# Kernel tuning notes

Hardware: AMD Instinct MI355X
Metric: run time of the kernel (lower is better)

Reference implementation:

```python
import jax, jax.numpy as jnp
import numpy as np

N_NODES = 50000
N_EDGES = 800000
N_GRAPHS = 500
IN_DIM = 128
HID = 96
OUT_DIM = 64


def _lin(k, fan_in, fan_out):
    return jax.random.normal(k, (fan_in, fan_out), jnp.float32) / np.float32(np.sqrt(fan_in))


def setup_inputs() -> dict:
    key = jax.random.key(0)
    ks = jax.random.split(key, 12)
    x = jax.random.normal(ks[0], (N_NODES, IN_DIM), jnp.float32)
    edge_index = jax.random.randint(ks[1], (2, N_EDGES), 0, N_NODES)
    batch = jnp.sort(jax.random.randint(ks[2], (N_NODES,), 0, N_GRAPHS))
    return {
        "x": x,
        "edge_index": edge_index,
        "batch": batch,
        # GCN conv weights (first: in->hid, rest: hid->hid)
        "W0": _lin(ks[3], IN_DIM, HID), "b0": jnp.zeros((HID,), jnp.float32),
        "W1": _lin(ks[4], HID, HID),    "b1": jnp.zeros((HID,), jnp.float32),
        "W2": _lin(ks[5], HID, HID),    "b2": jnp.zeros((HID,), jnp.float32),
        # jumping-knowledge 'cat' projection: 3*hid -> hid
        "Wjk": _lin(ks[6], 3 * HID, HID), "bjk": jnp.zeros((HID,), jnp.float32),
        # fc_o MLP: hid -> hid -> out
        "Wm1": _lin(ks[7], HID, HID),   "bm1": jnp.zeros((HID,), jnp.float32),
        "Wm2": _lin(ks[8], HID, OUT_DIM), "bm2": jnp.zeros((OUT_DIM,), jnp.float32),
    }


def reference(x, edge_index, batch, W0, b0, W1, b1, W2, b2, Wjk, bjk, Wm1, bm1, Wm2, bm2):
    n = x.shape[0]
    loop = jnp.arange(n, dtype=edge_index.dtype)
    src = jnp.concatenate([edge_index[0], loop])  # [E+N] with self-loops
    dst = jnp.concatenate([edge_index[1], loop])
    # symmetric GCN normalization: D^{-1/2} (A+I) D^{-1/2}
    deg = jax.ops.segment_sum(jnp.ones_like(dst, x.dtype), dst, num_segments=n)
    dinv = jax.lax.rsqrt(jnp.maximum(deg, 1.0))  # deg >= 1 with self-loops
    norm = dinv[src] * dinv[dst]  # [E+N]

    def gcn_conv(h, W, b):
        m = (h @ W)[src] * norm[:, None]                      # gather + scale
        return jax.ops.segment_sum(m, dst, num_segments=n) + b  # scatter-add

    h1 = jax.nn.relu(gcn_conv(x, W0, b0))
    h2 = jax.nn.relu(gcn_conv(h1, W1, b1))
    h3 = jax.nn.relu(gcn_conv(h2, W2, b2))
    # JK 'cat' + final linear (PyG BasicGNN lin)
    h = jnp.concatenate([h1, h2, h3], axis=-1) @ Wjk + bjk    # [N, HID]
    # global add pooling over graphs
    emb_o = jax.ops.segment_sum(h, batch, num_segments=N_GRAPHS)  # [G, HID]
    # fc_o MLP (eval: dropout/identity-batchnorm omitted)
    pred_o = jax.nn.relu(emb_o @ Wm1 + bm1) @ Wm2 + bm2       # [G, OUT]
    return pred_o
```

## Files before the change

### kernel.cpp

```cpp
#include <hip/hip_runtime.h>
#include <hip/hip_fp16.h>

#define NN 50000
#define NE 800000
#define NG 500
#define IND 128
#define HD 96
#define OD 64

#define SCAN_CHUNK 2048
#define SCAN_BLOCKS ((NN + SCAN_CHUNK - 1) / SCAN_CHUNK)


__global__ void zero_k(int* __restrict__ cnt) {
  int i = blockIdx.x * 256 + threadIdx.x;
  if (i < NN) cnt[i] = 0;
}

__global__ void hist_k(const int* __restrict__ dst, int* __restrict__ cnt,
                       int* __restrict__ rank) {
  int i0 = (blockIdx.x * 256 + threadIdx.x) * 8;
  if (i0 + 8 <= NE) {
    int4 d0 = *reinterpret_cast<const int4*>(&dst[i0]);
    int4 d1 = *reinterpret_cast<const int4*>(&dst[i0 + 4]);
    int4 r0, r1;
    r0.x = atomicAdd(&cnt[d0.x], 1);
    r0.y = atomicAdd(&cnt[d0.y], 1);
    r0.z = atomicAdd(&cnt[d0.z], 1);
    r0.w = atomicAdd(&cnt[d0.w], 1);
    r1.x = atomicAdd(&cnt[d1.x], 1);
    r1.y = atomicAdd(&cnt[d1.y], 1);
    r1.z = atomicAdd(&cnt[d1.z], 1);
    r1.w = atomicAdd(&cnt[d1.w], 1);
    *reinterpret_cast<int4*>(&rank[i0]) = r0;
    *reinterpret_cast<int4*>(&rank[i0 + 4]) = r1;
  } else {
    for (int i = i0; i < NE; i++) rank[i] = atomicAdd(&cnt[dst[i]], 1);
  }
}

__global__ void gstart_k(const int* __restrict__ batch, int* __restrict__ gstart) {
  int n = blockIdx.x * 256 + threadIdx.x;
  if (n >= NN) return;
  if (n == 0) {
    for (int g = 0; g <= batch[0]; g++) gstart[g] = 0;
    for (int g = batch[NN - 1] + 1; g <= NG; g++) gstart[g] = NN;
  } else {
    int b0 = batch[n - 1], b1 = batch[n];
    for (int g = b0 + 1; g <= b1; g++) gstart[g] = n;
  }
}

__global__ __launch_bounds__(256) void scan_part_k(const int* __restrict__ cnt,
                                                   int* __restrict__ bsum,
                                                   float* __restrict__ dinv) {
  __shared__ int ts[256];
  const int tid = threadIdx.x;
  const int base = blockIdx.x * SCAN_CHUNK + tid * 8;
  int s = 0;
#pragma unroll
  for (int j = 0; j < 8; j++) {
    int idx = base + j;
    if (idx < NN) {
      int c = cnt[idx];
      s += c;
      dinv[idx] = rsqrtf((float)(c + 1));
    }
  }
  ts[tid] = s;
  __syncthreads();
  for (int off = 128; off > 0; off >>= 1) {
    if (tid < off) ts[tid] += ts[tid + off];
    __syncthreads();
  }
  if (tid == 0) bsum[blockIdx.x] = ts[0];
}

__global__ __launch_bounds__(64) void scan_top_k(const int* __restrict__ bsum,
                                                 int* __restrict__ boff,
                                                 int* __restrict__ row_ptr) {
  int tid = threadIdx.x;
  int v = (tid < SCAN_BLOCKS) ? bsum[tid] : 0;
  for (int off = 1; off < 64; off <<= 1) {
    int u = __shfl_up(v, off);
    if (tid >= off) v += u;
  }
  if (tid < SCAN_BLOCKS) boff[tid] = v - bsum[tid];
  if (tid == 0) row_ptr[NN] = NE;
}

__global__ __launch_bounds__(256) void scan_fin_k(const int* __restrict__ cnt,
                                                  const int* __restrict__ boff,
                                                  int* __restrict__ row_ptr) {
  __shared__ int ts[256];
  const int tid = threadIdx.x;
  const int base = blockIdx.x * SCAN_CHUNK + tid * 8;
  int v[8];
  int s = 0;
#pragma unroll
  for (int j = 0; j < 8; j++) {
    int idx = base + j;
    v[j] = (idx < NN) ? cnt[idx] : 0;
    s += v[j];
  }
  ts[tid] = s;
  __syncthreads();
  for (int off = 1; off < 256; off <<= 1) {
    int t = (tid >= off) ? ts[tid - off] : 0;
    __syncthreads();
    ts[tid] += t;
    __syncthreads();
  }
  int run = ((tid == 0) ? 0 : ts[tid - 1]) + boff[blockIdx.x];
#pragma unroll
  for (int j = 0; j < 8; j++) {
    int idx = base + j;
    if (idx < NN) row_ptr[idx] = run;
    run += v[j];
  }
}

__global__ void fill_k(const int* __restrict__ src, const int* __restrict__ dst,
                       const int* __restrict__ row_ptr, const int* __restrict__ rank,
                       int* __restrict__ col) {
  int i0 = (blockIdx.x * 256 + threadIdx.x) * 8;
  if (i0 + 8 <= NE) {
    int4 d0 = *reinterpret_cast<const int4*>(&dst[i0]);
    int4 d1 = *reinterpret_cast<const int4*>(&dst[i0 + 4]);
    int4 s0 = *reinterpret_cast<const int4*>(&src[i0]);
    int4 s1 = *reinterpret_cast<const int4*>(&src[i0 + 4]);
    int4 r0 = *reinterpret_cast<const int4*>(&rank[i0]);
    int4 r1 = *reinterpret_cast<const int4*>(&rank[i0 + 4]);
    int p0 = row_ptr[d0.x], p1 = row_ptr[d0.y], p2 = row_ptr[d0.z], p3 = row_ptr[d0.w];
    int p4 = row_ptr[d1.x], p5 = row_ptr[d1.y], p6 = row_ptr[d1.z], p7 = row_ptr[d1.w];
    col[p0 + r0.x] = s0.x * (HD * 2);
    col[p1 + r0.y] = s0.y * (HD * 2);
    col[p2 + r0.z] = s0.z * (HD * 2);
    col[p3 + r0.w] = s0.w * (HD * 2);
    col[p4 + r1.x] = s1.x * (HD * 2);
    col[p5 + r1.y] = s1.y * (HD * 2);
    col[p6 + r1.z] = s1.z * (HD * 2);
    col[p7 + r1.w] = s1.w * (HD * 2);
  } else {
    for (int i = i0; i < NE; i++)
      col[row_ptr[dst[i]] + rank[i]] = src[i] * (HD * 2);
  }
}

template <int K, typename T>
__global__ __launch_bounds__(256) void gemm_scale_k(const T* __restrict__ h,
                                                    const float* __restrict__ W,
                                                    const float* __restrict__ dinv,
                                                    __half* __restrict__ g) {
  __shared__ float hsT[32][66];
  __shared__ __attribute__((aligned(16))) float ws[32][100];
  const int tid = threadIdx.x;
  const int rowg = tid >> 3;
  const int colg = tid & 7;
  const int row0 = blockIdx.x * 64;

  float acc[2][12];
#pragma unroll
  for (int i = 0; i < 2; i++)
#pragma unroll
    for (int j = 0; j < 12; j++) acc[i][j] = 0.f;

  for (int k0 = 0; k0 < K; k0 += 32) {
    if constexpr (sizeof(T) == 4) {
#pragma unroll
      for (int lin = tid; lin < 512; lin += 256) {
        int r = lin >> 3, q = lin & 7;
        int grow = row0 + r;
        float4 v = make_float4(0.f, 0.f, 0.f, 0.f);
        if (grow < NN)
          v = *reinterpret_cast<const float4*>(&h[(long)grow * K + k0 + 4 * q]);
        hsT[4 * q + 0][r] = v.x;
        hsT[4 * q + 1][r] = v.y;
        hsT[4 * q + 2][r] = v.z;
        hsT[4 * q + 3][r] = v.w;
      }
    } else {
      {
        int r = tid >> 2, q = tid & 3;
        int grow = row0 + r;
        if (grow < NN) {
          int4 raw = *reinterpret_cast<const int4*>(
              reinterpret_cast<const __half*>(h) + (long)grow * K + k0 + 8 * q);
          const __half2* hp = reinterpret_cast<const __half2*>(&raw);
#pragma unroll
          for (int t = 0; t < 4; t++) {
            float2 f = __half22float2(hp[t]);
            hsT[8 * q + 2 * t + 0][r] = f.x;
            hsT[8 * q + 2 * t + 1][r] = f.y;
          }
        } else {
#pragma unroll
          for (int t = 0; t < 8; t++) hsT[8 * q + t][r] = 0.f;
        }
      }
    }
#pragma unroll
    for (int lin = tid; lin < 768; lin += 256) {
      int kk = lin / 24, c4 = lin - kk * 24;
      *reinterpret_cast<float4*>(&ws[kk][4 * c4]) =
          *reinterpret_cast<const float4*>(&W[(long)(k0 + kk) * HD + 4 * c4]);
    }
    __syncthreads();
#pragma unroll 8
    for (int k = 0; k < 32; k++) {
      float2 a = *reinterpret_cast<const float2*>(&hsT[k][2 * rowg]);
      float4 w0 = *reinterpret_cast<const float4*>(&ws[k][12 * colg]);
      float4 w1 = *reinterpret_cast<const float4*>(&ws[k][12 * colg + 4]);
      float4 w2 = *reinterpret_cast<const float4*>(&ws[k][12 * colg + 8]);
      float wv[12] = {w0.x, w0.y, w0.z, w0.w, w1.x, w1.y, w1.z, w1.w,
                      w2.x, w2.y, w2.z, w2.w};
      float av[2] = {a.x, a.y};
#pragma unroll
      for (int i = 0; i < 2; i++)
#pragma unroll
        for (int j = 0; j < 12; j++) acc[i][j] = fmaf(av[i], wv[j], acc[i][j]);
    }
    __syncthreads();
  }
#pragma unroll
  for (int i = 0; i < 2; i++) {
    int row = row0 + 2 * rowg + i;
    if (row < NN) {
      float dv = dinv[row];
      __half2 hh[6];
#pragma unroll
      for (int q = 0; q < 6; q++)
        hh[q] = __floats2half2_rn(acc[i][2 * q] * dv, acc[i][2 * q + 1] * dv);
      __half* go = g + (long)row * HD + 12 * colg;
      *reinterpret_cast<float2*>(go) = *reinterpret_cast<float2*>(&hh[0]);
      *reinterpret_cast<float2*>(go + 4) = *reinterpret_cast<float2*>(&hh[2]);
      *reinterpret_cast<float2*>(go + 8) = *reinterpret_cast<float2*>(&hh[4]);
    }
  }
}

__global__ __launch_bounds__(256) void gather_k(const __half* __restrict__ g,
                                                const int* __restrict__ row_ptr,
                                                const int* __restrict__ col,
                                                const float* __restrict__ dinv,
                                                const float* __restrict__ bias,
                                                __half* __restrict__ hout) {
  int d = blockIdx.x * 4 + (threadIdx.x >> 6);
  int lane = threadIdx.x & 63;
  if (d >= NN) return;
  const bool active = (lane < 48);
  const int s = active ? (lane / 12) : 0;
  const int c = active ? (lane % 12) : 0;
  const int cofs = 16 * c;
  const char* gb = reinterpret_cast<const char*>(g);
  const int own = d * (HD * 2);

  float acc[8];
#pragma unroll
  for (int k = 0; k < 8; k++) acc[k] = 0.f;

  {
    float4 raw = *reinterpret_cast<const float4*>(gb + own + cofs);
    const __half2* hp = reinterpret_cast<const __half2*>(&raw);
    float m = (active && s == 0) ? 1.f : 0.f;
#pragma unroll
    for (int q = 0; q < 4; q++) {
      float2 f = __half22float2(hp[q]);
      acc[2 * q + 0] = fmaf(m, f.x, acc[2 * q + 0]);
      acc[2 * q + 1] = fmaf(m, f.y, acc[2 * q + 1]);
    }
  }

  int e = row_ptr[d];
  const int end = row_ptr[d + 1];
  while (e < end) {
    int cnt = end - e; if (cnt > 64) cnt = 64;
    int cid = (lane < cnt) ? col[e + lane] : own;
    int j = 0;
    for (; j + 16 <= cnt; j += 16) {
      int o0 = __shfl(cid, j + s);
      int o1 = __shfl(cid, j + 4 + s);
      int o2 = __shfl(cid, j + 8 + s);
      int o3 = __shfl(cid, j + 12 + s);
      float4 r0 = *reinterpret_cast<const float4*>(gb + o0 + cofs);
      float4 r1 = *reinterpret_cast<const float4*>(gb + o1 + cofs);
      float4 r2 = *reinterpret_cast<const float4*>(gb + o2 + cofs);
      float4 r3 = *reinterpret_cast<const float4*>(gb + o3 + cofs);
      const __half2* h0 = reinterpret_cast<const __half2*>(&r0);
      const __half2* h1 = reinterpret_cast<const __half2*>(&r1);
      const __half2* h2 = reinterpret_cast<const __half2*>(&r2);
      const __half2* h3 = reinterpret_cast<const __half2*>(&r3);
#pragma unroll
      for (int q = 0; q < 4; q++) {
        float2 f0 = __half22float2(h0[q]);
        float2 f1 = __half22float2(h1[q]);
        float2 f2 = __half22float2(h2[q]);
        float2 f3 = __half22float2(h3[q]);
        acc[2 * q + 0] += (f0.x + f1.x) + (f2.x + f3.x);
        acc[2 * q + 1] += (f0.y + f1.y) + (f2.y + f3.y);
      }
    }
    for (; j < cnt; j += 4) {
      int o = __shfl(cid, j + s);
      float m = (j + s < cnt) ? 1.f : 0.f;
      float4 r = *reinterpret_cast<const float4*>(gb + o + cofs);
      const __half2* hp = reinterpret_cast<const __half2*>(&r);
#pragma unroll
      for (int q = 0; q < 4; q++) {
        float2 f = __half22float2(hp[q]);
        acc[2 * q + 0] = fmaf(m, f.x, acc[2 * q + 0]);
        acc[2 * q + 1] = fmaf(m, f.y, acc[2 * q + 1]);
      }
    }
    e += 64;
  }

#pragma unroll
  for (int k = 0; k < 8; k++) acc[k] += __shfl(acc[k], lane + 24);
#pragma unroll
  for (int k = 0; k < 8; k++) acc[k] += __shfl(acc[k], lane + 12);

  if (lane < 12) {
    float dv = dinv[d];
    float4 b0 = *reinterpret_cast<const float4*>(&bias[8 * c]);
    float4 b1 = *reinterpret_cast<const float4*>(&bias[8 * c + 4]);
    float vb[8] = {b0.x, b0.y, b0.z, b0.w, b1.x, b1.y, b1.z, b1.w};
    __half2 hh[4];
#pragma unroll
    for (int q = 0; q < 4; q++) {
      float v0 = fmaxf(fmaf(acc[2 * q + 0], dv, vb[2 * q + 0]), 0.f);
      float v1 = fmaxf(fmaf(acc[2 * q + 1], dv, vb[2 * q + 1]), 0.f);
      hh[q] = __floats2half2_rn(v0, v1);
    }
    *reinterpret_cast<float4*>(&hout[(long)d * HD + 8 * c]) =
        *reinterpret_cast<float4*>(hh);
  }
}

__global__ __launch_bounds__(256) void pool3_k(const __half* __restrict__ hA,
                                               const __half* __restrict__ hB,
                                               const __half* __restrict__ hC,
                                               const int* __restrict__ gstart,
                                               float* __restrict__ P) {
  __shared__ float red[240][12];
  const int g = blockIdx.x;
  const int t = threadIdx.x;
  const int q = t % 24, s = t / 24;
  const int n0 = gstart[g], n1 = gstart[g + 1];
  if (t < 240) {
    float aA[4] = {0.f, 0.f, 0.f, 0.f}, aB[4] = {0.f, 0.f, 0.f, 0.f},
          aC[4] = {0.f, 0.f, 0.f, 0.f};
    for (int n = n0 + s; n < n1; n += 10) {
      float2 rA = *reinterpret_cast<const float2*>(&hA[(long)n * HD + 4 * q]);
      float2 rB = *reinterpret_cast<const float2*>(&hB[(long)n * HD + 4 * q]);
      float2 rC = *reinterpret_cast<const float2*>(&hC[(long)n * HD + 4 * q]);
      const __half2* pA = reinterpret_cast<const __half2*>(&rA);
      const __half2* pB = reinterpret_cast<const __half2*>(&rB);
      const __half2* pC = reinterpret_cast<const __half2*>(&rC);
#pragma unroll
      for (int u = 0; u < 2; u++) {
        float2 fA = __half22float2(pA[u]);
        float2 fB = __half22float2(pB[u]);
        float2 fC = __half22float2(pC[u]);
        aA[2 * u] += fA.x; aA[2 * u + 1] += fA.y;
        aB[2 * u] += fB.x; aB[2 * u + 1] += fB.y;
        aC[2 * u] += fC.x; aC[2 * u + 1] += fC.y;
      }
    }
#pragma unroll
    for (int u = 0; u < 4; u++) {
      red[t][u] = aA[u];
      red[t][4 + u] = aB[u];
      red[t][8 + u] = aC[u];
    }
  }
  __syncthreads();
  if (t < 24) {
    float sum[12];
#pragma unroll
    for (int u = 0; u < 12; u++) sum[u] = 0.f;
    for (int ss = 0; ss < 10; ss++)
#pragma unroll
      for (int u = 0; u < 12; u++) sum[u] += red[ss * 24 + t][u];
#pragma unroll
    for (int k = 0; k < 4; k++) {
      P[0 * NG * HD + g * HD + 4 * t + k] = sum[k];
      P[1 * NG * HD + g * HD + 4 * t + k] = sum[4 + k];
      P[2 * NG * HD + g * HD + 4 * t + k] = sum[8 + k];
    }
  }
}


__global__ void emb_k(const float* __restrict__ P, const int* __restrict__ gstart,
                      const float* __restrict__ Wjk, const float* __restrict__ bjk,
                      float* __restrict__ emb) {
  int idx = blockIdx.x * 256 + threadIdx.x;
  if (idx >= NG * HD) return;
  int gr = idx / HD, c = idx - gr * HD;
  const float* p1 = P + (long)gr * HD;
  const float* p2 = p1 + (long)NG * HD;
  const float* p3 = p2 + (long)NG * HD;
  float acc = (float)(gstart[gr + 1] - gstart[gr]) * bjk[c];
  for (int k = 0; k < HD; k++) {
    acc = fmaf(p1[k], Wjk[k * HD + c], acc);
    acc = fmaf(p2[k], Wjk[(HD + k) * HD + c], acc);
    acc = fmaf(p3[k], Wjk[(2 * HD + k) * HD + c], acc);
  }
  emb[idx] = acc;
}

__global__ void mlp1_k(const float* __restrict__ emb, const float* __restrict__ W,
                       const float* __restrict__ b, float* __restrict__ hid) {
  int idx = blockIdx.x * 256 + threadIdx.x;
  if (idx >= NG * HD) return;
  int gr = idx / HD, c = idx - gr * HD;
  const float* e = emb + (long)gr * HD;
  float acc = b[c];
  for (int k = 0; k < HD; k++) acc = fmaf(e[k], W[k * HD + c], acc);
  hid[idx] = fmaxf(acc, 0.f);
}

__global__ void mlp2_k(const float* __restrict__ hid, const float* __restrict__ W,
                       const float* __restrict__ b, float* __restrict__ out) {
  int idx = blockIdx.x * 256 + threadIdx.x;
  if (idx >= NG * OD) return;
  int gr = idx / OD, c = idx - gr * OD;
  const float* h = hid + (long)gr * HD;
  float acc = b[c];
  for (int k = 0; k < HD; k++) acc = fmaf(h[k], W[k * OD + c], acc);
  out[idx] = acc;
}


extern "C" void kernel_launch(void* const* d_in, const int* in_sizes, int n_in,
                              void* d_out, int out_size, void* d_ws, size_t ws_size,
                              hipStream_t stream) {
  const float* x = (const float*)d_in[0];
  const int* ei = (const int*)d_in[1];
  const int* batch = (const int*)d_in[2];
  const float* W0 = (const float*)d_in[3];  const float* b0 = (const float*)d_in[4];
  const float* W1 = (const float*)d_in[5];  const float* b1 = (const float*)d_in[6];
  const float* W2 = (const float*)d_in[7];  const float* b2 = (const float*)d_in[8];
  const float* Wjk = (const float*)d_in[9]; const float* bjk = (const float*)d_in[10];
  const float* Wm1 = (const float*)d_in[11]; const float* bm1 = (const float*)d_in[12];
  const float* Wm2 = (const float*)d_in[13]; const float* bm2 = (const float*)d_in[14];
  const int* srcp = ei;
  const int* dstp = ei + NE;

  char* wp = (char*)d_ws;
  size_t off = 0;
  auto alloc = [&](size_t bytes) -> void* {
    void* p = wp + off;
    off += bytes;
    off = (off + 255) & ~(size_t)255;
    return p;
  };
  int* cnt    = (int*)alloc((size_t)NN * 4);
  int* rowp   = (int*)alloc((size_t)(NN + 1) * 4);
  int* rank   = (int*)alloc((size_t)NE * 4);
  int* colb   = (int*)alloc((size_t)NE * 4);
  float* dinv = (float*)alloc((size_t)NN * 4);
  int* gstart = (int*)alloc((size_t)(NG + 1) * 4);
  int* bsum   = (int*)alloc((size_t)SCAN_BLOCKS * 4);
  int* boff   = (int*)alloc((size_t)SCAN_BLOCKS * 4);
  __half* g   = (__half*)alloc((size_t)NN * HD * 2);
  __half* hA  = (__half*)alloc((size_t)NN * HD * 2);
  __half* hB  = (__half*)alloc((size_t)NN * HD * 2);
  __half* hC  = (__half*)alloc((size_t)NN * HD * 2);
  float* P    = (float*)alloc((size_t)3 * NG * HD * 4);
  float* emb  = (float*)alloc((size_t)NG * HD * 4);
  float* hid  = (float*)alloc((size_t)NG * HD * 4);

  zero_k<<<(NN + 255) / 256, 256, 0, stream>>>(cnt);

  const int eb8 = (NE / 8 + 255) / 256;
  hist_k<<<eb8, 256, 0, stream>>>(dstp, cnt, rank);
  gstart_k<<<(NN + 255) / 256, 256, 0, stream>>>(batch, gstart);
  scan_part_k<<<SCAN_BLOCKS, 256, 0, stream>>>(cnt, bsum, dinv);
  scan_top_k<<<1, 64, 0, stream>>>(bsum, boff, rowp);
  scan_fin_k<<<SCAN_BLOCKS, 256, 0, stream>>>(cnt, boff, rowp);
  fill_k<<<eb8, 256, 0, stream>>>(srcp, dstp, rowp, rank, colb);

  const int gemm_grid = (NN + 63) / 64;
  const int gath_grid = (NN + 3) / 4;
  gemm_scale_k<IND, float><<<gemm_grid, 256, 0, stream>>>(x, W0, dinv, g);
  gather_k<<<gath_grid, 256, 0, stream>>>(g, rowp, colb, dinv, b0, hA);
  gemm_scale_k<HD, __half><<<gemm_grid, 256, 0, stream>>>(hA, W1, dinv, g);
  gather_k<<<gath_grid, 256, 0, stream>>>(g, rowp, colb, dinv, b1, hB);
  gemm_scale_k<HD, __half><<<gemm_grid, 256, 0, stream>>>(hB, W2, dinv, g);
  gather_k<<<gath_grid, 256, 0, stream>>>(g, rowp, colb, dinv, b2, hC);

  pool3_k<<<NG, 256, 0, stream>>>(hA, hB, hC, gstart, P);

  emb_k<<<(NG * HD + 255) / 256, 256, 0, stream>>>(P, gstart, Wjk, bjk, emb);
  mlp1_k<<<(NG * HD + 255) / 256, 256, 0, stream>>>(emb, Wm1, bm1, hid);
  mlp2_k<<<(NG * OD + 255) / 256, 256, 0, stream>>>(hid, Wm2, bm2, (float*)d_out);
}
```

Baseline: 252.0 us.

## Fuse pooling, JK projection and MLP head into one per-graph kernel

Merges the pooling, JK linear and two MLP kernels into a single per-graph block that keeps intermediates in shared memory. The graph-start kernel is dropped; each block binary-searches the sorted batch array to find its node range. This removes four launches and the global round-trips of the pooled and hidden buffers. In exchange, the small matvecs now run on at most 96 threads per block, and each block does redundant binary searches over batch.

```diff
diff --git a/kernel.cpp b/kernel.cpp
--- a/kernel.cpp
+++ b/kernel.cpp
@@ -36,18 +36,6 @@
     *reinterpret_cast<int4*>(&rank[i0 + 4]) = r1;
   } else {
     for (int i = i0; i < NE; i++) rank[i] = atomicAdd(&cnt[dst[i]], 1);
-  }
-}
-
-__global__ void gstart_k(const int* __restrict__ batch, int* __restrict__ gstart) {
-  int n = blockIdx.x * 256 + threadIdx.x;
-  if (n >= NN) return;
-  if (n == 0) {
-    for (int g = 0; g <= batch[0]; g++) gstart[g] = 0;
-    for (int g = batch[NN - 1] + 1; g <= NG; g++) gstart[g] = NN;
-  } else {
-    int b0 = batch[n - 1], b1 = batch[n];
-    for (int g = b0 + 1; g <= b1; g++) gstart[g] = n;
   }
 }
 
@@ -180,23 +168,21 @@
         hsT[4 * q + 3][r] = v.w;
       }
     } else {
-      {
-        int r = tid >> 2, q = tid & 3;
-        int grow = row0 + r;
-        if (grow < NN) {
-          int4 raw = *reinterpret_cast<const int4*>(
-              reinterpret_cast<const __half*>(h) + (long)grow * K + k0 + 8 * q);
-          const __half2* hp = reinterpret_cast<const __half2*>(&raw);
-#pragma unroll
-          for (int t = 0; t < 4; t++) {
-            float2 f = __half22float2(hp[t]);
-            hsT[8 * q + 2 * t + 0][r] = f.x;
-            hsT[8 * q + 2 * t + 1][r] = f.y;
-          }
-        } else {
-#pragma unroll
-          for (int t = 0; t < 8; t++) hsT[8 * q + t][r] = 0.f;
+      int r = tid >> 2, q = tid & 3;
+      int grow = row0 + r;
+      if (grow < NN) {
+        int4 raw = *reinterpret_cast<const int4*>(
+            reinterpret_cast<const __half*>(h) + (long)grow * K + k0 + 8 * q);
+        const __half2* hp = reinterpret_cast<const __half2*>(&raw);
+#pragma unroll
+        for (int t = 0; t < 4; t++) {
+          float2 f = __half22float2(hp[t]);
+          hsT[8 * q + 2 * t + 0][r] = f.x;
+          hsT[8 * q + 2 * t + 1][r] = f.y;
         }
+      } else {
+#pragma unroll
+        for (int t = 0; t < 8; t++) hsT[8 * q + t][r] = 0.f;
       }
     }
 #pragma unroll
@@ -337,16 +323,30 @@
   }
 }
 
-__global__ __launch_bounds__(256) void pool3_k(const __half* __restrict__ hA,
-                                               const __half* __restrict__ hB,
-                                               const __half* __restrict__ hC,
-                                               const int* __restrict__ gstart,
-                                               float* __restrict__ P) {
+__global__ __launch_bounds__(256) void head_k(const __half* __restrict__ hA,
+                                              const __half* __restrict__ hB,
+                                              const __half* __restrict__ hC,
+                                              const int* __restrict__ batch,
+                                              const float* __restrict__ Wjk,
+                                              const float* __restrict__ bjk,
+                                              const float* __restrict__ Wm1,
+                                              const float* __restrict__ bm1,
+                                              const float* __restrict__ Wm2,
+                                              const float* __restrict__ bm2,
+                                              float* __restrict__ out) {
   __shared__ float red[240][12];
+  __shared__ float p1[HD], p2[HD], p3[HD], se[HD], shid[HD];
   const int g = blockIdx.x;
   const int t = threadIdx.x;
+
+  int lo = 0, hi = NN;
+  while (lo < hi) { int mid = (lo + hi) >> 1; if (batch[mid] < g) lo = mid + 1; else hi = mid; }
+  const int n0 = lo;
+  lo = 0; hi = NN;
+  while (lo < hi) { int mid = (lo + hi) >> 1; if (batch[mid] < g + 1) lo = mid + 1; else hi = mid; }
+  const int n1 = lo;
+
   const int q = t % 24, s = t / 24;
-  const int n0 = gstart[g], n1 = gstart[g + 1];
   if (t < 240) {
     float aA[4] = {0.f, 0.f, 0.f, 0.f}, aB[4] = {0.f, 0.f, 0.f, 0.f},
           aC[4] = {0.f, 0.f, 0.f, 0.f};
@@ -384,52 +384,34 @@
       for (int u = 0; u < 12; u++) sum[u] += red[ss * 24 + t][u];
 #pragma unroll
     for (int k = 0; k < 4; k++) {
-      P[0 * NG * HD + g * HD + 4 * t + k] = sum[k];
-      P[1 * NG * HD + g * HD + 4 * t + k] = sum[4 + k];
-      P[2 * NG * HD + g * HD + 4 * t + k] = sum[8 + k];
-    }
-  }
-}
-
-
-__global__ void emb_k(const float* __restrict__ P, const int* __restrict__ gstart,
-                      const float* __restrict__ Wjk, const float* __restrict__ bjk,
-                      float* __restrict__ emb) {
-  int idx = blockIdx.x * 256 + threadIdx.x;
-  if (idx >= NG * HD) return;
-  int gr = idx / HD, c = idx - gr * HD;
-  const float* p1 = P + (long)gr * HD;
-  const float* p2 = p1 + (long)NG * HD;
-  const float* p3 = p2 + (long)NG * HD;
-  float acc = (float)(gstart[gr + 1] - gstart[gr]) * bjk[c];
-  for (int k = 0; k < HD; k++) {
-    acc = fmaf(p1[k], Wjk[k * HD + c], acc);
-    acc = fmaf(p2[k], Wjk[(HD + k) * HD + c], acc);
-    acc = fmaf(p3[k], Wjk[(2 * HD + k) * HD + c], acc);
-  }
-  emb[idx] = acc;
-}
-
-__global__ void mlp1_k(const float* __restrict__ emb, const float* __restrict__ W,
-                       const float* __restrict__ b, float* __restrict__ hid) {
-  int idx = blockIdx.x * 256 + threadIdx.x;
-  if (idx >= NG * HD) return;
-  int gr = idx / HD, c = idx - gr * HD;
-  const float* e = emb + (long)gr * HD;
-  float acc = b[c];
-  for (int k = 0; k < HD; k++) acc = fmaf(e[k], W[k * HD + c], acc);
-  hid[idx] = fmaxf(acc, 0.f);
-}
-
-__global__ void mlp2_k(const float* __restrict__ hid, const float* __restrict__ W,
-                       const float* __restrict__ b, float* __restrict__ out) {
-  int idx = blockIdx.x * 256 + threadIdx.x;
-  if (idx >= NG * OD) return;
-  int gr = idx / OD, c = idx - gr * OD;
-  const float* h = hid + (long)gr * HD;
-  float acc = b[c];
-  for (int k = 0; k < HD; k++) acc = fmaf(h[k], W[k * OD + c], acc);
-  out[idx] = acc;
+      p1[4 * t + k] = sum[k];
+      p2[4 * t + k] = sum[4 + k];
+      p3[4 * t + k] = sum[8 + k];
+    }
+  }
+  __syncthreads();
+
+  if (t < HD) {
+    float acc = (float)(n1 - n0) * bjk[t];
+    for (int k = 0; k < HD; k++) {
+      acc = fmaf(p1[k], Wjk[k * HD + t], acc);
+      acc = fmaf(p2[k], Wjk[(HD + k) * HD + t], acc);
+      acc = fmaf(p3[k], Wjk[(2 * HD + k) * HD + t], acc);
+    }
+    se[t] = acc;
+  }
+  __syncthreads();
+  if (t < HD) {
+    float acc = bm1[t];
+    for (int k = 0; k < HD; k++) acc = fmaf(se[k], Wm1[k * HD + t], acc);
+    shid[t] = fmaxf(acc, 0.f);
+  }
+  __syncthreads();
+  if (t < OD) {
+    float acc = bm2[t];
+    for (int k = 0; k < HD; k++) acc = fmaf(shid[k], Wm2[k * OD + t], acc);
+    out[g * OD + t] = acc;
+  }
 }
 
 
@@ -461,22 +443,17 @@
   int* rank   = (int*)alloc((size_t)NE * 4);
   int* colb   = (int*)alloc((size_t)NE * 4);
   float* dinv = (float*)alloc((size_t)NN * 4);
-  int* gstart = (int*)alloc((size_t)(NG + 1) * 4);
   int* bsum   = (int*)alloc((size_t)SCAN_BLOCKS * 4);
   int* boff   = (int*)alloc((size_t)SCAN_BLOCKS * 4);
   __half* g   = (__half*)alloc((size_t)NN * HD * 2);
   __half* hA  = (__half*)alloc((size_t)NN * HD * 2);
   __half* hB  = (__half*)alloc((size_t)NN * HD * 2);
   __half* hC  = (__half*)alloc((size_t)NN * HD * 2);
-  float* P    = (float*)alloc((size_t)3 * NG * HD * 4);
-  float* emb  = (float*)alloc((size_t)NG * HD * 4);
-  float* hid  = (float*)alloc((size_t)NG * HD * 4);
 
   zero_k<<<(NN + 255) / 256, 256, 0, stream>>>(cnt);
 
   const int eb8 = (NE / 8 + 255) / 256;
   hist_k<<<eb8, 256, 0, stream>>>(dstp, cnt, rank);
-  gstart_k<<<(NN + 255) / 256, 256, 0, stream>>>(batch, gstart);
   scan_part_k<<<SCAN_BLOCKS, 256, 0, stream>>>(cnt, bsum, dinv);
   scan_top_k<<<1, 64, 0, stream>>>(bsum, boff, rowp);
   scan_fin_k<<<SCAN_BLOCKS, 256, 0, stream>>>(cnt, boff, rowp);
@@ -491,9 +468,6 @@
   gemm_scale_k<HD, __half><<<gemm_grid, 256, 0, stream>>>(hB, W2, dinv, g);
   gather_k<<<gath_grid, 256, 0, stream>>>(g, rowp, colb, dinv, b2, hC);
 
-  pool3_k<<<NG, 256, 0, stream>>>(hA, hB, hC, gstart, P);
-
-  emb_k<<<(NG * HD + 255) / 256, 256, 0, stream>>>(P, gstart, Wjk, bjk, emb);
-  mlp1_k<<<(NG * HD + 255) / 256, 256, 0, stream>>>(emb, Wm1, bm1, hid);
-  mlp2_k<<<(NG * OD + 255) / 256, 256, 0, stream>>>(hid, Wm2, bm2, (float*)d_out);
-}
+  head_k<<<NG, 256, 0, stream>>>(hA, hB, hC, batch, Wjk, bjk, Wm1, bm1, Wm2, bm2,
+                                 (float*)d_out);
+}
```

New measurement: 240.1 us. -4.7%, faster.
